# Optimization experiments

Measured on AMD Instinct MI355X. Metric: run time of the kernel, lower is better.

## Reference

```python
import jax, jax.numpy as jnp
import numpy as np


def _gcn_conv(x, W, b, src, dst, n_nodes):
    # PyG GCNConv with add_self_loops=True, edge_weight=None (implicit ones),
    # symmetric normalization: D^{-1/2} A_hat D^{-1/2} (X W) + b
    xw = x @ W                                    # [N, H]
    loop = jnp.arange(n_nodes, dtype=src.dtype)
    src_f = jnp.concatenate([src, loop])          # [E+N]
    dst_f = jnp.concatenate([dst, loop])          # [E+N]
    w = jnp.ones(src_f.shape[0], dtype=x.dtype)
    deg = jax.ops.segment_sum(w, dst_f, num_segments=n_nodes)  # in-degree incl. self-loop
    dinv = jnp.where(deg > 0, jax.lax.rsqrt(deg), 0.0)
    norm = dinv[src_f] * dinv[dst_f]              # [E+N]
    msgs = norm[:, None] * xw[src_f]              # [E+N, H]
    out = jax.ops.segment_sum(msgs, dst_f, num_segments=n_nodes)
    return out + b


def setup_inputs() -> dict:
    key = jax.random.key(0)
    k1, k2, k3, k4 = jax.random.split(key, 4)
    N, E, D, H = 100000, 1600000, 256, 128
    x = jax.random.normal(k1, (N, D), dtype=jnp.float32)
    edge_index = jax.random.randint(k2, (2, E), 0, N, dtype=jnp.int64)
    # Glorot-scaled weights
    W1 = jax.random.normal(k3, (D, H), dtype=jnp.float32) * np.sqrt(2.0 / (D + H))
    b1 = jnp.zeros((H,), dtype=jnp.float32)
    W2 = jax.random.normal(k4, (H, 1), dtype=jnp.float32) * np.sqrt(2.0 / (H + 1))
    b2 = jnp.zeros((1,), dtype=jnp.float32)
    return {"x": x, "edge_index": edge_index, "W1": W1, "b1": b1, "W2": W2, "b2": b2}


def reference(x, edge_index, W1, b1, W2, b2):
    n_nodes = x.shape[0]
    src, dst = edge_index[0], edge_index[1]
    h = _gcn_conv(x, W1, b1, src, dst, n_nodes)   # conv1
    h = jax.nn.relu(h)                            # relu; dropout is identity in eval mode
    out = _gcn_conv(h, W2, b2, src, dst, n_nodes) # conv2 -> [N, 1]
    return out.reshape(-1)                        # x.view(-1)
```

## Files before the change

kernel.cpp:

```cpp
#include <hip/hip_runtime.h>
#include <hip/hip_fp16.h>
#include <cstdint>
#include <cstddef>


#define ELLW 64

typedef _Float16 half8 __attribute__((ext_vector_type(8)));
typedef _Float16 half2t __attribute__((ext_vector_type(2)));
typedef float floatx4 __attribute__((ext_vector_type(4)));

__global__ __launch_bounds__(256) void wswz_k(const float* __restrict__ W1,
                                              _Float16* __restrict__ wz) {
  int id = blockIdx.x * 256 + threadIdx.x;
  int j = id & 7, lane = (id >> 3) & 63, nb = (id >> 9) & 7, kb = id >> 12;
  int k = kb * 32 + ((lane >> 4) << 3) + j;
  int n = nb * 16 + (lane & 15);
  wz[id] = (_Float16)W1[k * 128 + n];
}

__global__ __launch_bounds__(256) void fused_k(const float* __restrict__ X,
                                               const _Float16* __restrict__ wz,
                                               _Float16* __restrict__ z1h, int N,
                                               const int* __restrict__ src,
                                               const int* __restrict__ dst,
                                               int* __restrict__ cnt,
                                               int* __restrict__ ell, int E,
                                               int gb) {
  __shared__ char lds_raw[32 * 1024];

  if (blockIdx.x >= gb) {
    int base = ((blockIdx.x - gb) * 256 + threadIdx.x) * 4;
    if (base + 3 < E) {
      int4 d4 = *(const int4*)(dst + base);
      int4 s4 = *(const int4*)(src + base);
      int p0 = atomicAdd(&cnt[d4.x], 1);
      int p1 = atomicAdd(&cnt[d4.y], 1);
      int p2 = atomicAdd(&cnt[d4.z], 1);
      int p3 = atomicAdd(&cnt[d4.w], 1);
      if (p0 < ELLW) ell[(size_t)d4.x * ELLW + p0] = s4.x;
      if (p1 < ELLW) ell[(size_t)d4.y * ELLW + p1] = s4.y;
      if (p2 < ELLW) ell[(size_t)d4.z * ELLW + p2] = s4.z;
      if (p3 < ELLW) ell[(size_t)d4.w * ELLW + p3] = s4.w;
    } else {
      for (int e = base; e < E && e < base + 4; ++e) {
        int d = dst[e];
        int p = atomicAdd(&cnt[d], 1);
        if (p < ELLW) ell[(size_t)d * ELLW + p] = src[e];
      }
    }
    return;
  }

  _Float16* Bl = (_Float16*)lds_raw;
  _Float16* Ol = (_Float16*)lds_raw;

  int tid = threadIdx.x;
  int wave = tid >> 6, lane = tid & 63;
  int m = lane & 15, q = lane >> 4;
  int row0 = blockIdx.x * 64;
  int row = row0 + wave * 16 + m;

  floatx4 acc[8];
#pragma unroll
  for (int nb = 0; nb < 8; ++nb) acc[nb] = (floatx4)(0.f);

  const uint4* wsrc = (const uint4*)wz;
  uint4* bdst = (uint4*)Bl;

#pragma unroll
  for (int ph = 0; ph < 2; ++ph) {
    if (ph) __syncthreads();
#pragma unroll
    for (int i = 0; i < 8; ++i) bdst[i * 256 + tid] = wsrc[ph * 2048 + i * 256 + tid];
    __syncthreads();
#pragma unroll
    for (int kk = 0; kk < 4; ++kk) {
      int kb = ph * 4 + kk;
      half8 a;
      if (row < N) {
        const float* ap = X + (size_t)row * 256 + kb * 32 + q * 8;
        float4 a0 = *(const float4*)ap;
        float4 a1 = *(const float4*)(ap + 4);
        a[0] = (_Float16)a0.x; a[1] = (_Float16)a0.y;
        a[2] = (_Float16)a0.z; a[3] = (_Float16)a0.w;
        a[4] = (_Float16)a1.x; a[5] = (_Float16)a1.y;
        a[6] = (_Float16)a1.z; a[7] = (_Float16)a1.w;
      } else {
#pragma unroll
        for (int j = 0; j < 8; ++j) a[j] = (_Float16)0.f;
      }
#pragma unroll
      for (int nb = 0; nb < 8; ++nb) {
        half8 b = *(const half8*)(Bl + ((size_t)(kk * 8 + nb) * 64 + lane) * 8);
        acc[nb] = __builtin_amdgcn_mfma_f32_16x16x32_f16(a, b, acc[nb], 0, 0, 0);
      }
    }
  }
  __syncthreads();

#pragma unroll
  for (int nb = 0; nb < 8; ++nb) {
    int col = nb * 16 + m;
#pragma unroll
    for (int r = 0; r < 4; ++r) {
      int orow = wave * 16 + q * 4 + r;
      Ol[orow * 128 + col] = (_Float16)acc[nb][r];
    }
  }
  __syncthreads();

  const uint4* osrc = (const uint4*)Ol;
  uint4* gdst = (uint4*)(z1h + (size_t)row0 * 128);
#pragma unroll
  for (int i = 0; i < 4; ++i) {
    int idx = i * 256 + tid;
    int r = idx >> 4;
    if (row0 + r < N) gdst[idx] = osrc[idx];
  }
}

__global__ __launch_bounds__(256) void prep2_k(const int* __restrict__ cnt,
                                               float* __restrict__ dinv,
                                               _Float16* __restrict__ z1h,
                                               float* __restrict__ z2w,
                                               int N, int nd) {
  int b = blockIdx.x, tid = threadIdx.x;
  if (b < nd) {
    int i = b * 256 + tid;
    if (i < N) dinv[i] = rsqrtf((float)(cnt[i] + 1));
  } else {
    if (tid < 128) z1h[(size_t)N * 128 + tid] = (_Float16)0.f;
    if (tid == 0) { z2w[N] = 0.f; dinv[N] = 0.f; }
  }
}

__global__ __launch_bounds__(256) void agg1_k(const _Float16* __restrict__ z1h,
                                              const float* __restrict__ dinv,
                                              const int* __restrict__ cnt,
                                              const int* __restrict__ ell,
                                              const float* __restrict__ b1,
                                              const float* __restrict__ W2,
                                              float* __restrict__ z2w, int N) {
  int d = blockIdx.x * 4 + (threadIdx.x >> 6);
  int lane = threadIdx.x & 63;
  if (d >= N) return;
  int c = min(cnt[d], ELLW);
  int idx = (lane < c) ? ell[(size_t)d * ELLW + lane] : N;
  float wl = dinv[idx];
  float dd = dinv[d];

  half2t self = ((const half2t*)(z1h + (size_t)d * 128))[lane];
  float ax = dd * (float)self[0];
  float ay = dd * (float)self[1];

  int cpad = (c + 7) & ~7;
  for (int e = 0; e < cpad; e += 8) {
#pragma unroll
    for (int j = 0; j < 8; ++j) {
      int s = __builtin_amdgcn_readlane(idx, e + j);
      float w = __int_as_float(__builtin_amdgcn_readlane(__float_as_int(wl), e + j));
      half2t v = ((const half2t*)(z1h + (size_t)s * 128))[lane];
      ax = fmaf(w, (float)v[0], ax);
      ay = fmaf(w, (float)v[1], ay);
    }
  }

  float2 bb = ((const float2*)b1)[lane];
  float hx = fmaxf(fmaf(dd, ax, bb.x), 0.f);
  float hy = fmaxf(fmaf(dd, ay, bb.y), 0.f);
  float2 w2 = ((const float2*)W2)[lane];
  float dot = hx * w2.x + hy * w2.y;
#pragma unroll
  for (int off = 32; off >= 1; off >>= 1) dot += __shfl_xor(dot, off, 64);
  if (lane == 0) z2w[d] = dd * dot;
}

__global__ __launch_bounds__(256) void agg2_k(const float* __restrict__ z2w,
                                              const float* __restrict__ dinv,
                                              const int* __restrict__ cnt,
                                              const int* __restrict__ ell,
                                              const float* __restrict__ b2,
                                              float* __restrict__ out, int N) {
  int d = blockIdx.x * 4 + (threadIdx.x >> 6);
  int lane = threadIdx.x & 63;
  if (d >= N) return;
  int c = min(cnt[d], ELLW);
  int idx = (lane < c) ? ell[(size_t)d * ELLW + lane] : N;
  float v = z2w[idx];
#pragma unroll
  for (int off = 32; off >= 1; off >>= 1) v += __shfl_xor(v, off, 64);
  if (lane == 0) out[d] = dinv[d] * (v + z2w[d]) + b2[0];
}

extern "C" void kernel_launch(void* const* d_in, const int* in_sizes, int n_in,
                              void* d_out, int out_size, void* d_ws, size_t ws_size,
                              hipStream_t stream) {
  (void)n_in; (void)out_size; (void)ws_size;
  const float* x = (const float*)d_in[0];
  const int* edge = (const int*)d_in[1];
  const float* W1 = (const float*)d_in[2];
  const float* b1 = (const float*)d_in[3];
  const float* W2 = (const float*)d_in[4];
  const float* b2 = (const float*)d_in[5];
  float* out = (float*)d_out;

  const int D = 256, H = 128;
  int N = in_sizes[0] / D;
  int E = in_sizes[1] / 2;
  const int* srcp = edge;
  const int* dstp = edge + E;

  char* ws = (char*)d_ws;
  size_t off = 0;
  auto alloc = [&](size_t bytes) -> void* {
    void* p = ws + off;
    off += (bytes + 255) & ~(size_t)255;
    return p;
  };
  int* cnt        = (int*)alloc((size_t)N * 4);
  float* dinv     = (float*)alloc((size_t)(N + 1) * 4);
  float* z2w      = (float*)alloc((size_t)(N + 1) * 4);
  int* ell        = (int*)alloc((size_t)N * ELLW * 4);
  _Float16* wz    = (_Float16*)alloc((size_t)32768 * 2);
  _Float16* z1h   = (_Float16*)alloc((size_t)(N + 1) * H * 2);

  hipMemsetAsync(cnt, 0, (size_t)N * 4, stream);

  int gb = (N + 63) / 64;
  int fb = (E + 1023) / 1024;
  int nd = (N + 255) / 256;
  wswz_k<<<dim3(128), dim3(256), 0, stream>>>(W1, wz);
  fused_k<<<dim3(gb + fb), dim3(256), 0, stream>>>(x, wz, z1h, N, srcp, dstp, cnt, ell, E, gb);
  prep2_k<<<dim3(nd + 1), dim3(256), 0, stream>>>(cnt, dinv, z1h, z2w, N, nd);
  agg1_k<<<dim3((N + 3) / 4), dim3(256), 0, stream>>>(z1h, dinv, cnt, ell, b1, W2, z2w, N);
  agg2_k<<<dim3((N + 3) / 4), dim3(256), 0, stream>>>(z2w, dinv, cnt, ell, b2, out, N);
}
```

Measured before the change: 322.0 us.

## Merge prep kernels, compute degree norms inline, widen edge batching and unroll

Folds the count memset, the W1 swizzle and the sentinel-row init into a single prep kernel. It drops the separate dinv pass by recomputing rsqrt(cnt+1) inside both aggregation kernels. Each edge-bucketing thread now handles 8 edges instead of 4, and the GEMM stages W in four 16KB LDS phases instead of two 32KB ones. It also adds nontemporal loads for X, edges and ELL rows, and unrolls the gather loop by 16. The aim is fewer launches and less global traffic; the cost is redundant rsqrt work, extra cnt gathers, and more padding lanes in the gather loop.

```diff
diff --git a/kernel.cpp b/kernel.cpp
--- a/kernel.cpp
+++ b/kernel.cpp
@@ -9,14 +9,30 @@
 typedef _Float16 half8 __attribute__((ext_vector_type(8)));
 typedef _Float16 half2t __attribute__((ext_vector_type(2)));
 typedef float floatx4 __attribute__((ext_vector_type(4)));
-
-__global__ __launch_bounds__(256) void wswz_k(const float* __restrict__ W1,
-                                              _Float16* __restrict__ wz) {
-  int id = blockIdx.x * 256 + threadIdx.x;
-  int j = id & 7, lane = (id >> 3) & 63, nb = (id >> 9) & 7, kb = id >> 12;
-  int k = kb * 32 + ((lane >> 4) << 3) + j;
-  int n = nb * 16 + (lane & 15);
-  wz[id] = (_Float16)W1[k * 128 + n];
+typedef float floatv4 __attribute__((ext_vector_type(4)));
+typedef int intv4 __attribute__((ext_vector_type(4)));
+typedef unsigned int uintv4 __attribute__((ext_vector_type(4)));
+
+__global__ __launch_bounds__(256) void prep0_k(int* __restrict__ cnt,
+                                               const float* __restrict__ W1,
+                                               _Float16* __restrict__ wz,
+                                               _Float16* __restrict__ z1h,
+                                               float* __restrict__ z2w,
+                                               int N, int nd) {
+  int b = blockIdx.x, tid = threadIdx.x;
+  if (b < nd) {
+    int i = b * 256 + tid;
+    if (i <= N) cnt[i] = 0;
+  } else if (b < nd + 128) {
+    int id = (b - nd) * 256 + tid;
+    int j = id & 7, lane = (id >> 3) & 63, nb = (id >> 9) & 7, kb = id >> 12;
+    int k = kb * 32 + ((lane >> 4) << 3) + j;
+    int n = nb * 16 + (lane & 15);
+    wz[id] = (_Float16)W1[k * 128 + n];
+  } else {
+    if (tid < 128) z1h[(size_t)N * 128 + tid] = (_Float16)0.f;
+    if (tid == 0) z2w[N] = 0.f;
+  }
 }
 
 __global__ __launch_bounds__(256) void fused_k(const float* __restrict__ X,
@@ -27,26 +43,28 @@
                                                int* __restrict__ cnt,
                                                int* __restrict__ ell, int E,
                                                int gb) {
-  __shared__ char lds_raw[32 * 1024];
+  __shared__ char lds_raw[16 * 1024];
 
   if (blockIdx.x >= gb) {
-    int base = ((blockIdx.x - gb) * 256 + threadIdx.x) * 4;
-    if (base + 3 < E) {
-      int4 d4 = *(const int4*)(dst + base);
-      int4 s4 = *(const int4*)(src + base);
-      int p0 = atomicAdd(&cnt[d4.x], 1);
-      int p1 = atomicAdd(&cnt[d4.y], 1);
-      int p2 = atomicAdd(&cnt[d4.z], 1);
-      int p3 = atomicAdd(&cnt[d4.w], 1);
-      if (p0 < ELLW) ell[(size_t)d4.x * ELLW + p0] = s4.x;
-      if (p1 < ELLW) ell[(size_t)d4.y * ELLW + p1] = s4.y;
-      if (p2 < ELLW) ell[(size_t)d4.z * ELLW + p2] = s4.z;
-      if (p3 < ELLW) ell[(size_t)d4.w * ELLW + p3] = s4.w;
+    int base = ((blockIdx.x - gb) * 256 + threadIdx.x) * 8;
+    if (base + 7 < E) {
+      intv4 d0 = __builtin_nontemporal_load((const intv4*)(dst + base));
+      intv4 d1 = __builtin_nontemporal_load((const intv4*)(dst + base + 4));
+      intv4 s0 = __builtin_nontemporal_load((const intv4*)(src + base));
+      intv4 s1 = __builtin_nontemporal_load((const intv4*)(src + base + 4));
+      int d[8] = {d0[0], d0[1], d0[2], d0[3], d1[0], d1[1], d1[2], d1[3]};
+      int s[8] = {s0[0], s0[1], s0[2], s0[3], s1[0], s1[1], s1[2], s1[3]};
+      int p[8];
+#pragma unroll
+      for (int i = 0; i < 8; ++i) p[i] = atomicAdd(&cnt[d[i]], 1);
+#pragma unroll
+      for (int i = 0; i < 8; ++i)
+        if (p[i] < ELLW) ell[(size_t)d[i] * ELLW + p[i]] = s[i];
     } else {
-      for (int e = base; e < E && e < base + 4; ++e) {
-        int d = dst[e];
-        int p = atomicAdd(&cnt[d], 1);
-        if (p < ELLW) ell[(size_t)d * ELLW + p] = src[e];
+      for (int e = base; e < E && e < base + 8; ++e) {
+        int dd = dst[e];
+        int p = atomicAdd(&cnt[dd], 1);
+        if (p < ELLW) ell[(size_t)dd * ELLW + p] = src[e];
       }
     }
     return;
@@ -65,27 +83,27 @@
 #pragma unroll
   for (int nb = 0; nb < 8; ++nb) acc[nb] = (floatx4)(0.f);
 
-  const uint4* wsrc = (const uint4*)wz;
-  uint4* bdst = (uint4*)Bl;
-
-#pragma unroll
-  for (int ph = 0; ph < 2; ++ph) {
+  const uintv4* wsrc = (const uintv4*)wz;
+  uintv4* bdst = (uintv4*)Bl;
+
+#pragma unroll
+  for (int ph = 0; ph < 4; ++ph) {
     if (ph) __syncthreads();
 #pragma unroll
-    for (int i = 0; i < 8; ++i) bdst[i * 256 + tid] = wsrc[ph * 2048 + i * 256 + tid];
+    for (int i = 0; i < 4; ++i) bdst[i * 256 + tid] = wsrc[ph * 1024 + i * 256 + tid];
     __syncthreads();
 #pragma unroll
-    for (int kk = 0; kk < 4; ++kk) {
-      int kb = ph * 4 + kk;
+    for (int kk = 0; kk < 2; ++kk) {
+      int kb = ph * 2 + kk;
       half8 a;
       if (row < N) {
-        const float* ap = X + (size_t)row * 256 + kb * 32 + q * 8;
-        float4 a0 = *(const float4*)ap;
-        float4 a1 = *(const float4*)(ap + 4);
-        a[0] = (_Float16)a0.x; a[1] = (_Float16)a0.y;
-        a[2] = (_Float16)a0.z; a[3] = (_Float16)a0.w;
-        a[4] = (_Float16)a1.x; a[5] = (_Float16)a1.y;
-        a[6] = (_Float16)a1.z; a[7] = (_Float16)a1.w;
+        const floatv4* ap = (const floatv4*)(X + (size_t)row * 256 + kb * 32 + q * 8);
+        floatv4 a0 = __builtin_nontemporal_load(ap);
+        floatv4 a1 = __builtin_nontemporal_load(ap + 1);
+        a[0] = (_Float16)a0[0]; a[1] = (_Float16)a0[1];
+        a[2] = (_Float16)a0[2]; a[3] = (_Float16)a0[3];
+        a[4] = (_Float16)a1[0]; a[5] = (_Float16)a1[1];
+        a[6] = (_Float16)a1[2]; a[7] = (_Float16)a1[3];
       } else {
 #pragma unroll
         for (int j = 0; j < 8; ++j) a[j] = (_Float16)0.f;
@@ -110,8 +128,8 @@
   }
   __syncthreads();
 
-  const uint4* osrc = (const uint4*)Ol;
-  uint4* gdst = (uint4*)(z1h + (size_t)row0 * 128);
+  const uintv4* osrc = (const uintv4*)Ol;
+  uintv4* gdst = (uintv4*)(z1h + (size_t)row0 * 128);
 #pragma unroll
   for (int i = 0; i < 4; ++i) {
     int idx = i * 256 + tid;
@@ -120,23 +138,7 @@
   }
 }
 
-__global__ __launch_bounds__(256) void prep2_k(const int* __restrict__ cnt,
-                                               float* __restrict__ dinv,
-                                               _Float16* __restrict__ z1h,
-                                               float* __restrict__ z2w,
-                                               int N, int nd) {
-  int b = blockIdx.x, tid = threadIdx.x;
-  if (b < nd) {
-    int i = b * 256 + tid;
-    if (i < N) dinv[i] = rsqrtf((float)(cnt[i] + 1));
-  } else {
-    if (tid < 128) z1h[(size_t)N * 128 + tid] = (_Float16)0.f;
-    if (tid == 0) { z2w[N] = 0.f; dinv[N] = 0.f; }
-  }
-}
-
 __global__ __launch_bounds__(256) void agg1_k(const _Float16* __restrict__ z1h,
-                                              const float* __restrict__ dinv,
                                               const int* __restrict__ cnt,
                                               const int* __restrict__ ell,
                                               const float* __restrict__ b1,
@@ -145,19 +147,21 @@
   int d = blockIdx.x * 4 + (threadIdx.x >> 6);
   int lane = threadIdx.x & 63;
   if (d >= N) return;
-  int c = min(cnt[d], ELLW);
-  int idx = (lane < c) ? ell[(size_t)d * ELLW + lane] : N;
-  float wl = dinv[idx];
-  float dd = dinv[d];
+  int cd = cnt[d];
+  int c = min(cd, ELLW);
+  int raw = __builtin_nontemporal_load(ell + (size_t)d * ELLW + lane);
+  int idx = (lane < c) ? raw : N;
+  float wl = rsqrtf((float)(cnt[idx] + 1));
+  float dd = rsqrtf((float)(cd + 1));
 
   half2t self = ((const half2t*)(z1h + (size_t)d * 128))[lane];
   float ax = dd * (float)self[0];
   float ay = dd * (float)self[1];
 
-  int cpad = (c + 7) & ~7;
-  for (int e = 0; e < cpad; e += 8) {
-#pragma unroll
-    for (int j = 0; j < 8; ++j) {
+  int cpad = (c + 15) & ~15;
+  for (int e = 0; e < cpad; e += 16) {
+#pragma unroll
+    for (int j = 0; j < 16; ++j) {
       int s = __builtin_amdgcn_readlane(idx, e + j);
       float w = __int_as_float(__builtin_amdgcn_readlane(__float_as_int(wl), e + j));
       half2t v = ((const half2t*)(z1h + (size_t)s * 128))[lane];
@@ -177,7 +181,6 @@
 }
 
 __global__ __launch_bounds__(256) void agg2_k(const float* __restrict__ z2w,
-                                              const float* __restrict__ dinv,
                                               const int* __restrict__ cnt,
                                               const int* __restrict__ ell,
                                               const float* __restrict__ b2,
@@ -185,12 +188,14 @@
   int d = blockIdx.x * 4 + (threadIdx.x >> 6);
   int lane = threadIdx.x & 63;
   if (d >= N) return;
-  int c = min(cnt[d], ELLW);
-  int idx = (lane < c) ? ell[(size_t)d * ELLW + lane] : N;
+  int cd = cnt[d];
+  int c = min(cd, ELLW);
+  int raw = __builtin_nontemporal_load(ell + (size_t)d * ELLW + lane);
+  int idx = (lane < c) ? raw : N;
   float v = z2w[idx];
 #pragma unroll
   for (int off = 32; off >= 1; off >>= 1) v += __shfl_xor(v, off, 64);
-  if (lane == 0) out[d] = dinv[d] * (v + z2w[d]) + b2[0];
+  if (lane == 0) out[d] = rsqrtf((float)(cd + 1)) * (v + z2w[d]) + b2[0];
 }
 
 extern "C" void kernel_launch(void* const* d_in, const int* in_sizes, int n_in,
@@ -218,21 +223,17 @@
     off += (bytes + 255) & ~(size_t)255;
     return p;
   };
-  int* cnt        = (int*)alloc((size_t)N * 4);
-  float* dinv     = (float*)alloc((size_t)(N + 1) * 4);
+  int* cnt        = (int*)alloc((size_t)(N + 1) * 4);
   float* z2w      = (float*)alloc((size_t)(N + 1) * 4);
   int* ell        = (int*)alloc((size_t)N * ELLW * 4);
   _Float16* wz    = (_Float16*)alloc((size_t)32768 * 2);
   _Float16* z1h   = (_Float16*)alloc((size_t)(N + 1) * H * 2);
 
-  hipMemsetAsync(cnt, 0, (size_t)N * 4, stream);
-
   int gb = (N + 63) / 64;
-  int fb = (E + 1023) / 1024;
-  int nd = (N + 255) / 256;
-  wswz_k<<<dim3(128), dim3(256), 0, stream>>>(W1, wz);
+  int fb = (E + 2047) / 2048;
+  int nd = (N + 256) / 256;
+  prep0_k<<<dim3(nd + 128 + 1), dim3(256), 0, stream>>>(cnt, W1, wz, z1h, z2w, N, nd);
   fused_k<<<dim3(gb + fb), dim3(256), 0, stream>>>(x, wz, z1h, N, srcp, dstp, cnt, ell, E, gb);
-  prep2_k<<<dim3(nd + 1), dim3(256), 0, stream>>>(cnt, dinv, z1h, z2w, N, nd);
-  agg1_k<<<dim3((N + 3) / 4), dim3(256), 0, stream>>>(z1h, dinv, cnt, ell, b1, W2, z2w, N);
-  agg2_k<<<dim3((N + 3) / 4), dim3(256), 0, stream>>>(z2w, dinv, cnt, ell, b2, out, N);
-}
+  agg1_k<<<dim3((N + 3) / 4), dim3(256), 0, stream>>>(z1h, cnt, ell, b1, W2, z2w, N);
+  agg2_k<<<dim3((N + 3) / 4), dim3(256), 0, stream>>>(z2w, cnt, ell, b2, out, N);
+}
```

Measured after the change: 325.7 us. Within noise of the previous version (+1.1%).
